# Kernel tuning notes

Hardware: AMD Instinct MI355X
Metric: run time of the kernel (lower is better)

The kernel has to match this reference:

```python
import jax, jax.numpy as jnp
import numpy as np

DIM = 512        # token feature dim
HID = 1024       # expert hidden dim (dim * 2)
E = 16           # num_experts
N = 8192         # num tokens
TOPK = 2         # experts active per token (routing sparsity)


def setup_inputs() -> dict:
    key = jax.random.key(0)
    k_x, k_s, k_w1, k_w2 = jax.random.split(key, 4)
    x = jax.random.normal(k_x, (N, DIM), dtype=jnp.float32)
    # sparse routing scores: top-2 experts per token get nonzero score, rest 0
    scores = jax.random.uniform(k_s, (N, E), dtype=jnp.float32)
    vals, idx = jax.lax.top_k(scores, TOPK)
    routing_tensor = jnp.zeros((N, E), jnp.float32).at[jnp.arange(N)[:, None], idx].set(vals)
    # per-expert MLP params (depth=2, bias=True): Linear(DIM->HID), GELU, Linear(HID->DIM)
    W1 = jax.random.normal(k_w1, (E, DIM, HID), dtype=jnp.float32) * (1.0 / np.sqrt(DIM))
    b1 = jnp.zeros((E, HID), jnp.float32)
    W2 = jax.random.normal(k_w2, (E, HID, DIM), dtype=jnp.float32) * (1.0 / np.sqrt(HID))
    b2 = jnp.zeros((E, DIM), jnp.float32)
    return {"x": x, "routing_tensor": routing_tensor, "W1": W1, "b1": b1, "W2": W2, "b2": b2}


def reference(x, routing_tensor, W1, b1, W2, b2):
    # out[n] = sum_e routing[n,e] * MLP_e(x[n]); rows with score 0 contribute 0,
    # which is exactly the original mask-gather / scatter-add semantics.
    h = jax.nn.gelu(jnp.einsum('nd,edh->enh', x, W1) + b1[:, None, :], approximate=False)
    y = jnp.einsum('enh,ehd->end', h, W2) + b2[:, None, :]  # [E, N, DIM]
    return jnp.einsum('end,ne->nd', y, routing_tensor)       # combine weighted by scores
```

## Files before the change

### kernel.cpp

```cpp
#include <hip/hip_runtime.h>
#include <hip/hip_bf16.h>

#define NTOK 8192
#define DIM 512
#define HID 1024
#define NE 16
#define CAP 1280
#define MT 20

typedef __attribute__((ext_vector_type(8))) short short8;
typedef __attribute__((ext_vector_type(8))) unsigned short us8;
typedef __attribute__((ext_vector_type(4))) float f32x4;

static __device__ __forceinline__ unsigned short f2bf(float f) {
    __hip_bfloat16 h = __float2bfloat16(f);
    return __builtin_bit_cast(unsigned short, h);
}
static __device__ __forceinline__ float bf2f(unsigned short u) {
    unsigned int v = (unsigned int)u << 16;
    return __builtin_bit_cast(float, v);
}

static __device__ __forceinline__ void gl_lds16(const unsigned short* g, unsigned short* l) {
    __builtin_amdgcn_global_load_lds(
        (const __attribute__((address_space(1))) unsigned int*)g,
        (__attribute__((address_space(3))) unsigned int*)l, 16, 0, 0);
}

static __device__ __forceinline__ float gelu_f(float v) {
    float u = v * (0.7978845608f + 0.0356774081f * v * v);
    return v / (1.0f + __expf(-2.0f * u));
}

__global__ __launch_bounds__(256) void route_fill(const float* __restrict__ routing,
                                                  int* __restrict__ cnt,
                                                  int* __restrict__ sidx,
                                                  float* __restrict__ wtb) {
    __shared__ int lcnt[NE], lbase[NE];
    int t = threadIdx.x;
    int n = blockIdx.x * 256 + t;
    if (t < NE) lcnt[t] = 0;
    __syncthreads();
    int mye[2]; float myw[2]; int mypos[2]; int slot = 0;
    #pragma unroll
    for (int e = 0; e < NE; e++) {
        float r = routing[n * NE + e];
        if (r != 0.0f && slot < 2) {
            mye[slot] = e; myw[slot] = r;
            mypos[slot] = atomicAdd(&lcnt[e], 1);
            slot++;
        }
    }
    __syncthreads();
    if (t < NE) lbase[t] = atomicAdd(&cnt[t], lcnt[t]);
    __syncthreads();
    for (int s = 0; s < slot; s++) {
        int e = mye[s];
        int p = lbase[e] + mypos[s];
        if (p < CAP) { sidx[e * CAP + p] = n * 2 + s; wtb[e * CAP + p] = myw[s]; }
    }
}

__global__ __launch_bounds__(256) void prep2(const float* __restrict__ W1,
                                             const float* __restrict__ W2,
                                             unsigned short* __restrict__ w1t,
                                             unsigned short* __restrict__ w2t,
                                             const float* __restrict__ x,
                                             const int* __restrict__ cnt,
                                             const int* __restrict__ sidx,
                                             unsigned short* __restrict__ xg) {
    int b = blockIdx.x;
    int t = threadIdx.x;
    if (b < 4096) {
        __shared__ float tile[64][65];
        const float* src; unsigned short* dst; int R, C, bx, by;
        if (b < 2048) {
            int e = b >> 7, rem = b & 127; bx = rem & 15; by = rem >> 4;
            R = DIM; C = HID;
            src = W1 + (size_t)e * R * C; dst = w1t + (size_t)e * R * C;
        } else {
            int bb = b - 2048;
            int e = bb >> 7, rem = bb & 127; bx = rem & 7; by = rem >> 3;
            R = HID; C = DIM;
            src = W2 + (size_t)e * R * C; dst = w2t + (size_t)e * R * C;
        }
        int c0 = bx * 64, r0 = by * 64;
        int tx = t & 15, ty = t >> 4;
        #pragma unroll
        for (int i = 0; i < 4; i++) {
            float4 v = *(const float4*)(src + (size_t)(r0 + ty + i * 16) * C + c0 + tx * 4);
            tile[ty + i * 16][tx * 4 + 0] = v.x;
            tile[ty + i * 16][tx * 4 + 1] = v.y;
            tile[ty + i * 16][tx * 4 + 2] = v.z;
            tile[ty + i * 16][tx * 4 + 3] = v.w;
        }
        __syncthreads();
        int seg = t & 7;
        #pragma unroll
        for (int i = 0; i < 2; i++) {
            int dr = (t >> 3) + i * 32;
            us8 o;
            #pragma unroll
            for (int j = 0; j < 8; j++)
                o[j] = f2bf(tile[seg * 8 + j][dr]);
            *(us8*)(dst + (size_t)(c0 + dr) * R + r0 + seg * 8) = o;
        }
    } else {
        int gi = b - 4096;
        int lane = t & 63, rl = t >> 6;
        int row = gi * 4 + rl;
        int e = row / CAP, r = row - e * CAP;
        int c = cnt[e]; c = c > CAP ? CAP : c;
        us8 o;
        if (r < c) {
            int n = sidx[row] >> 1;
            const float* xr = x + (size_t)n * DIM + lane * 8;
            float4 v0 = *(const float4*)xr;
            float4 v1 = *(const float4*)(xr + 4);
            o[0] = f2bf(v0.x); o[1] = f2bf(v0.y); o[2] = f2bf(v0.z); o[3] = f2bf(v0.w);
            o[4] = f2bf(v1.x); o[5] = f2bf(v1.y); o[6] = f2bf(v1.z); o[7] = f2bf(v1.w);
        } else {
            #pragma unroll
            for (int j = 0; j < 8; j++) o[j] = 0;
        }
        *(us8*)(xg + (size_t)row * DIM + lane * 8) = o;
    }
}

template <int K>
__device__ __forceinline__ void mfma_main64(const unsigned short* __restrict__ A,
                                            const unsigned short* __restrict__ B,
                                            unsigned short* As, unsigned short* Bs,
                                            f32x4 acc[2][4]) {
    int t = threadIdx.x;
    int wave = t >> 6, lane = t & 63;
    int wm = wave >> 1, wn = wave & 1;
    int quad = lane >> 4, l16 = lane & 15;
    int lr = lane >> 3;
    int col = (lane & 7) << 3;
    for (int kc = 0; kc < K; kc += 64) {
        __syncthreads();
        #pragma unroll
        for (int j = 0; j < 2; j++) {
            int rb = wave * 16 + j * 8;
            gl_lds16(A + (size_t)(rb + lr) * K + kc + col, As + rb * 64);
        }
        #pragma unroll
        for (int j = 0; j < 4; j++) {
            int rb = wave * 32 + j * 8;
            gl_lds16(B + (size_t)(rb + lr) * K + kc + col, Bs + rb * 64);
        }
        __syncthreads();
        #pragma unroll
        for (int kk = 0; kk < 64; kk += 32) {
            short8 av[2], bv[4];
            #pragma unroll
            for (int mt = 0; mt < 2; mt++)
                av[mt] = *(const short8*)(&As[(wm * 32 + mt * 16 + l16) * 64 + kk + quad * 8]);
            #pragma unroll
            for (int nt = 0; nt < 4; nt++)
                bv[nt] = *(const short8*)(&Bs[(wn * 64 + nt * 16 + l16) * 64 + kk + quad * 8]);
            #pragma unroll
            for (int mt = 0; mt < 2; mt++)
                #pragma unroll
                for (int nt = 0; nt < 4; nt++)
                    acc[mt][nt] = __builtin_amdgcn_mfma_f32_16x16x32_bf16(
                        av[mt], bv[nt], acc[mt][nt], 0, 0, 0);
        }
    }
}


__global__ __launch_bounds__(256, 5) void gemm1_gelu(
    const unsigned short* __restrict__ xg, const unsigned short* __restrict__ w1t,
    const float* __restrict__ b1, const int* __restrict__ cnt,
    unsigned short* __restrict__ hbuf) {
    __shared__ __align__(16) unsigned short As[64 * 64];
    __shared__ __align__(16) unsigned short Bs[128 * 64];
    int L = blockIdx.x;
    int cc = L & 7, n = (L >> 3) & 7, g = L >> 6;
    int pi = cc + (g << 3);
    int e = pi / MT, m = pi % MT;
    int c = cnt[e]; c = c > CAP ? CAP : c;
    int m0 = m * 64;
    if (m0 >= c) return;
    int n0 = n * 128;
    const unsigned short* A = xg + ((size_t)e * CAP + m0) * DIM;
    const unsigned short* B = w1t + ((size_t)e * HID + n0) * DIM;
    f32x4 z = {0.f, 0.f, 0.f, 0.f};
    f32x4 acc[2][4];
    #pragma unroll
    for (int mt = 0; mt < 2; mt++)
        #pragma unroll
        for (int nt = 0; nt < 4; nt++) acc[mt][nt] = z;
    mfma_main64<DIM>(A, B, As, Bs, acc);
    int t = threadIdx.x;
    int wave = t >> 6, lane = t & 63;
    int wm = wave >> 1, wn = wave & 1, quad = lane >> 4, l16 = lane & 15;
    #pragma unroll
    for (int nt = 0; nt < 4; nt++) {
        int gn = n0 + wn * 64 + nt * 16 + l16;
        float bias = b1[e * HID + gn];
        #pragma unroll
        for (int mt = 0; mt < 2; mt++) {
            #pragma unroll
            for (int r = 0; r < 4; r++) {
                int gm = m0 + wm * 32 + mt * 16 + quad * 4 + r;
                float v = acc[mt][nt][r] + bias;
                hbuf[((size_t)e * CAP + gm) * HID + gn] = f2bf(gelu_f(v));
            }
        }
    }
}

__global__ __launch_bounds__(256, 5) void gemm2_store(
    const unsigned short* __restrict__ hbuf, const unsigned short* __restrict__ w2t,
    const float* __restrict__ b2, const int* __restrict__ cnt,
    const int* __restrict__ sidx, const float* __restrict__ wtb,
    unsigned short* __restrict__ ybuf) {
    __shared__ __align__(16) unsigned short As[64 * 64];
    __shared__ __align__(16) unsigned short Bs[128 * 64];
    int L = blockIdx.x;
    int cc = L & 7, n = (L >> 3) & 3, g = L >> 5;
    int pi = cc + (g << 3);
    int e = pi / MT, m = pi % MT;
    int c = cnt[e]; c = c > CAP ? CAP : c;
    int m0 = m * 64;
    if (m0 >= c) return;
    int n0 = n * 128;
    const unsigned short* A = hbuf + ((size_t)e * CAP + m0) * HID;
    const unsigned short* B = w2t + ((size_t)e * DIM + n0) * HID;
    f32x4 z = {0.f, 0.f, 0.f, 0.f};
    f32x4 acc[2][4];
    #pragma unroll
    for (int mt = 0; mt < 2; mt++)
        #pragma unroll
        for (int nt = 0; nt < 4; nt++) acc[mt][nt] = z;
    mfma_main64<HID>(A, B, As, Bs, acc);
    int t = threadIdx.x;
    int wave = t >> 6, lane = t & 63;
    int wm = wave >> 1, wn = wave & 1, quad = lane >> 4, l16 = lane & 15;
    float b2v[4];
    #pragma unroll
    for (int nt = 0; nt < 4; nt++)
        b2v[nt] = b2[e * DIM + n0 + wn * 64 + nt * 16 + l16];
    #pragma unroll
    for (int mt = 0; mt < 2; mt++) {
        #pragma unroll
        for (int r = 0; r < 4; r++) {
            int gm = m0 + wm * 32 + mt * 16 + quad * 4 + r;
            if (gm < c) {
                int si = sidx[e * CAP + gm];
                float wgt = wtb[e * CAP + gm];
                unsigned short* yrow = ybuf + (size_t)si * DIM;
                #pragma unroll
                for (int nt = 0; nt < 4; nt++) {
                    int gn = n0 + wn * 64 + nt * 16 + l16;
                    yrow[gn] = f2bf(wgt * (acc[mt][nt][r] + b2v[nt]));
                }
            }
        }
    }
}

__global__ void combine(const unsigned short* __restrict__ yb, float* __restrict__ out) {
    int i = blockIdx.x * 256 + threadIdx.x;
    int n = i >> 6, d8 = i & 63;
    us8 a = ((const us8*)(yb + (size_t)(2 * n) * DIM))[d8];
    us8 b = ((const us8*)(yb + (size_t)(2 * n + 1) * DIM))[d8];
    float4 o0, o1;
    o0.x = bf2f(a[0]) + bf2f(b[0]); o0.y = bf2f(a[1]) + bf2f(b[1]);
    o0.z = bf2f(a[2]) + bf2f(b[2]); o0.w = bf2f(a[3]) + bf2f(b[3]);
    o1.x = bf2f(a[4]) + bf2f(b[4]); o1.y = bf2f(a[5]) + bf2f(b[5]);
    o1.z = bf2f(a[6]) + bf2f(b[6]); o1.w = bf2f(a[7]) + bf2f(b[7]);
    float* op = out + (size_t)n * DIM + d8 * 8;
    *(float4*)op = o0;
    *(float4*)(op + 4) = o1;
}

extern "C" void kernel_launch(void* const* d_in, const int* in_sizes, int n_in,
                              void* d_out, int out_size, void* d_ws, size_t ws_size,
                              hipStream_t stream) {
    const float* x       = (const float*)d_in[0];
    const float* routing = (const float*)d_in[1];
    const float* W1      = (const float*)d_in[2];
    const float* b1      = (const float*)d_in[3];
    const float* W2      = (const float*)d_in[4];
    const float* b2      = (const float*)d_in[5];
    float* out = (float*)d_out;

    char* w = (char*)d_ws;
    int*   cnt  = (int*)w;
    int*   sidx = (int*)(w + 256);
    float* wtb  = (float*)(w + 256 + NE * CAP * 4);
    char* base = w + 256 + NE * CAP * 8;
    unsigned short* xg  = (unsigned short*)base;
    unsigned short* hb  = xg + (size_t)NE * CAP * DIM;
    unsigned short* w1t = hb + (size_t)NE * CAP * HID;
    unsigned short* w2t = w1t + (size_t)NE * HID * DIM;
    unsigned short* ybuf = w2t + (size_t)NE * DIM * HID;

    hipMemsetAsync(cnt, 0, 256, stream);

    route_fill<<<NTOK / 256, 256, 0, stream>>>(routing, cnt, sidx, wtb);
    prep2<<<4096 + 5120, 256, 0, stream>>>(W1, W2, w1t, w2t, x, cnt, sidx, xg);

    gemm1_gelu<<<8 * MT * NE, 256, 0, stream>>>(xg, w1t, b1, cnt, hb);
    gemm2_store<<<4 * MT * NE, 256, 0, stream>>>(hb, w2t, b2, cnt, sidx, wtb, ybuf);
    combine<<<(NTOK * DIM / 8) / 256, 256, 0, stream>>>(ybuf, out);
}
```

Before: 220.0 us.

## Fuse memset, routing and prep into one cooperative persistent kernel

Replaces the memset plus the route_fill and prep2 launches with a single cooperative kernel of 1024 persistent blocks that zero the counters, build routing lists, then transpose weights and gather tokens, separated by grid-wide syncs. The aim is to remove launch overhead and inter-kernel gaps. In exchange it adds grid.sync costs, and the grid-stride loop may give the transpose and gather phase lower occupancy and parallelism. Cooperative launch also needs all 1024 blocks to be resident at once.

```diff
diff --git a/kernel.cpp b/kernel.cpp
--- a/kernel.cpp
+++ b/kernel.cpp
@@ -1,5 +1,8 @@
 #include <hip/hip_runtime.h>
 #include <hip/hip_bf16.h>
+#include <hip/hip_cooperative_groups.h>
+
+namespace cg = cooperative_groups;
 
 #define NTOK 8192
 #define DIM 512
@@ -32,98 +35,101 @@
     return v / (1.0f + __expf(-2.0f * u));
 }
 
-__global__ __launch_bounds__(256) void route_fill(const float* __restrict__ routing,
-                                                  int* __restrict__ cnt,
-                                                  int* __restrict__ sidx,
-                                                  float* __restrict__ wtb) {
+__global__ __launch_bounds__(256, 4) void prep_coop(
+    const float* __restrict__ routing, int* __restrict__ cnt,
+    int* __restrict__ sidx, float* __restrict__ wtb,
+    const float* __restrict__ W1, const float* __restrict__ W2,
+    unsigned short* __restrict__ w1t, unsigned short* __restrict__ w2t,
+    const float* __restrict__ x, unsigned short* __restrict__ xg) {
+    cg::grid_group grid = cg::this_grid();
+    __shared__ float tile[64][65];
     __shared__ int lcnt[NE], lbase[NE];
     int t = threadIdx.x;
-    int n = blockIdx.x * 256 + t;
-    if (t < NE) lcnt[t] = 0;
-    __syncthreads();
-    int mye[2]; float myw[2]; int mypos[2]; int slot = 0;
-    #pragma unroll
-    for (int e = 0; e < NE; e++) {
-        float r = routing[n * NE + e];
-        if (r != 0.0f && slot < 2) {
-            mye[slot] = e; myw[slot] = r;
-            mypos[slot] = atomicAdd(&lcnt[e], 1);
-            slot++;
-        }
-    }
-    __syncthreads();
-    if (t < NE) lbase[t] = atomicAdd(&cnt[t], lcnt[t]);
-    __syncthreads();
-    for (int s = 0; s < slot; s++) {
-        int e = mye[s];
-        int p = lbase[e] + mypos[s];
-        if (p < CAP) { sidx[e * CAP + p] = n * 2 + s; wtb[e * CAP + p] = myw[s]; }
-    }
-}
-
-__global__ __launch_bounds__(256) void prep2(const float* __restrict__ W1,
-                                             const float* __restrict__ W2,
-                                             unsigned short* __restrict__ w1t,
-                                             unsigned short* __restrict__ w2t,
-                                             const float* __restrict__ x,
-                                             const int* __restrict__ cnt,
-                                             const int* __restrict__ sidx,
-                                             unsigned short* __restrict__ xg) {
-    int b = blockIdx.x;
-    int t = threadIdx.x;
-    if (b < 4096) {
-        __shared__ float tile[64][65];
-        const float* src; unsigned short* dst; int R, C, bx, by;
-        if (b < 2048) {
-            int e = b >> 7, rem = b & 127; bx = rem & 15; by = rem >> 4;
-            R = DIM; C = HID;
-            src = W1 + (size_t)e * R * C; dst = w1t + (size_t)e * R * C;
+    int nb = gridDim.x;
+
+    if (blockIdx.x == 0 && t < NE) cnt[t] = 0;
+    grid.sync();
+
+    for (int u = blockIdx.x; u < NTOK / 256; u += nb) {
+        int n = u * 256 + t;
+        if (t < NE) lcnt[t] = 0;
+        __syncthreads();
+        int mye[2]; float myw[2]; int mypos[2]; int slot = 0;
+        #pragma unroll
+        for (int e = 0; e < NE; e++) {
+            float r = routing[n * NE + e];
+            if (r != 0.0f && slot < 2) {
+                mye[slot] = e; myw[slot] = r;
+                mypos[slot] = atomicAdd(&lcnt[e], 1);
+                slot++;
+            }
+        }
+        __syncthreads();
+        if (t < NE) lbase[t] = atomicAdd(&cnt[t], lcnt[t]);
+        __syncthreads();
+        for (int s = 0; s < slot; s++) {
+            int e = mye[s];
+            int p = lbase[e] + mypos[s];
+            if (p < CAP) { sidx[e * CAP + p] = n * 2 + s; wtb[e * CAP + p] = myw[s]; }
+        }
+    }
+    grid.sync();
+
+    for (int u = blockIdx.x; u < 9216; u += nb) {
+        if (u < 4096) {
+            const float* src; unsigned short* dst; int R, C, bx, by;
+            if (u < 2048) {
+                int e = u >> 7, rem = u & 127; bx = rem & 15; by = rem >> 4;
+                R = DIM; C = HID;
+                src = W1 + (size_t)e * R * C; dst = w1t + (size_t)e * R * C;
+            } else {
+                int bb = u - 2048;
+                int e = bb >> 7, rem = bb & 127; bx = rem & 7; by = rem >> 3;
+                R = HID; C = DIM;
+                src = W2 + (size_t)e * R * C; dst = w2t + (size_t)e * R * C;
+            }
+            int c0 = bx * 64, r0 = by * 64;
+            int tx = t & 15, ty = t >> 4;
+            __syncthreads();
+            #pragma unroll
+            for (int i = 0; i < 4; i++) {
+                float4 v = *(const float4*)(src + (size_t)(r0 + ty + i * 16) * C + c0 + tx * 4);
+                tile[ty + i * 16][tx * 4 + 0] = v.x;
+                tile[ty + i * 16][tx * 4 + 1] = v.y;
+                tile[ty + i * 16][tx * 4 + 2] = v.z;
+                tile[ty + i * 16][tx * 4 + 3] = v.w;
+            }
+            __syncthreads();
+            int seg = t & 7;
+            #pragma unroll
+            for (int i = 0; i < 2; i++) {
+                int dr = (t >> 3) + i * 32;
+                us8 o;
+                #pragma unroll
+                for (int j = 0; j < 8; j++)
+                    o[j] = f2bf(tile[seg * 8 + j][dr]);
+                *(us8*)(dst + (size_t)(c0 + dr) * R + r0 + seg * 8) = o;
+            }
         } else {
-            int bb = b - 2048;
-            int e = bb >> 7, rem = bb & 127; bx = rem & 7; by = rem >> 3;
-            R = HID; C = DIM;
-            src = W2 + (size_t)e * R * C; dst = w2t + (size_t)e * R * C;
-        }
-        int c0 = bx * 64, r0 = by * 64;
-        int tx = t & 15, ty = t >> 4;
-        #pragma unroll
-        for (int i = 0; i < 4; i++) {
-            float4 v = *(const float4*)(src + (size_t)(r0 + ty + i * 16) * C + c0 + tx * 4);
-            tile[ty + i * 16][tx * 4 + 0] = v.x;
-            tile[ty + i * 16][tx * 4 + 1] = v.y;
-            tile[ty + i * 16][tx * 4 + 2] = v.z;
-            tile[ty + i * 16][tx * 4 + 3] = v.w;
-        }
-        __syncthreads();
-        int seg = t & 7;
-        #pragma unroll
-        for (int i = 0; i < 2; i++) {
-            int dr = (t >> 3) + i * 32;
+            int gi = u - 4096;
+            int lane = t & 63, rl = t >> 6;
+            int row = gi * 4 + rl;
+            int e = row / CAP, r = row - e * CAP;
+            int c = cnt[e]; c = c > CAP ? CAP : c;
             us8 o;
-            #pragma unroll
-            for (int j = 0; j < 8; j++)
-                o[j] = f2bf(tile[seg * 8 + j][dr]);
-            *(us8*)(dst + (size_t)(c0 + dr) * R + r0 + seg * 8) = o;
-        }
-    } else {
-        int gi = b - 4096;
-        int lane = t & 63, rl = t >> 6;
-        int row = gi * 4 + rl;
-        int e = row / CAP, r = row - e * CAP;
-        int c = cnt[e]; c = c > CAP ? CAP : c;
-        us8 o;
-        if (r < c) {
-            int n = sidx[row] >> 1;
-            const float* xr = x + (size_t)n * DIM + lane * 8;
-            float4 v0 = *(const float4*)xr;
-            float4 v1 = *(const float4*)(xr + 4);
-            o[0] = f2bf(v0.x); o[1] = f2bf(v0.y); o[2] = f2bf(v0.z); o[3] = f2bf(v0.w);
-            o[4] = f2bf(v1.x); o[5] = f2bf(v1.y); o[6] = f2bf(v1.z); o[7] = f2bf(v1.w);
-        } else {
-            #pragma unroll
-            for (int j = 0; j < 8; j++) o[j] = 0;
-        }
-        *(us8*)(xg + (size_t)row * DIM + lane * 8) = o;
+            if (r < c) {
+                int n = sidx[row] >> 1;
+                const float* xr = x + (size_t)n * DIM + lane * 8;
+                float4 v0 = *(const float4*)xr;
+                float4 v1 = *(const float4*)(xr + 4);
+                o[0] = f2bf(v0.x); o[1] = f2bf(v0.y); o[2] = f2bf(v0.z); o[3] = f2bf(v0.w);
+                o[4] = f2bf(v1.x); o[5] = f2bf(v1.y); o[6] = f2bf(v1.z); o[7] = f2bf(v1.w);
+            } else {
+                #pragma unroll
+                for (int j = 0; j < 8; j++) o[j] = 0;
+            }
+            *(us8*)(xg + (size_t)row * DIM + lane * 8) = o;
+        }
     }
 }
 
@@ -300,10 +306,10 @@
     unsigned short* w2t = w1t + (size_t)NE * HID * DIM;
     unsigned short* ybuf = w2t + (size_t)NE * DIM * HID;
 
-    hipMemsetAsync(cnt, 0, 256, stream);
-
-    route_fill<<<NTOK / 256, 256, 0, stream>>>(routing, cnt, sidx, wtb);
-    prep2<<<4096 + 5120, 256, 0, stream>>>(W1, W2, w1t, w2t, x, cnt, sidx, xg);
+    void* args[] = {(void*)&routing, (void*)&cnt, (void*)&sidx, (void*)&wtb,
+                    (void*)&W1, (void*)&W2, (void*)&w1t, (void*)&w2t,
+                    (void*)&x, (void*)&xg};
+    hipLaunchCooperativeKernel((void*)prep_coop, dim3(1024), dim3(256), args, 0, stream);
 
     gemm1_gelu<<<8 * MT * NE, 256, 0, stream>>>(xg, w1t, b1, cnt, hb);
     gemm2_store<<<4 * MT * NE, 256, 0, stream>>>(hb, w2t, b2, cnt, sidx, wtb, ybuf);
```

Result: slower. 389.2 us (+76.9%).
